# Kernel optimization log

Measured on AMD Instinct MI355X. Metric: run time of the kernel, lower is better.

## Reference

```python
import jax, jax.numpy as jnp
import numpy as np

B, N, K, D = 4096, 64, 48, 64   # batch, n_features, n_bins, d_embedding
F = N * D                        # flattened embedding dim
E, H, O = 8, 1024, 512           # experts, expert hidden, expert out
T, TH = 2, 256                   # tasks, tower hidden


def setup_inputs() -> dict:
    key = jax.random.key(0)
    ks = jax.random.split(key, 10)
    # PLE buffers from uniform bins linspace(0,1,K+1): w = 1/width, b = -edge/width
    edges = jnp.linspace(0.0, 1.0, K + 1)
    width = jnp.diff(edges)
    w = 1.0 / width                      # (K,)
    b = -edges[:-1] / width              # (K,)
    ple_weight = jnp.broadcast_to(w, (N, K)).astype(jnp.float32)
    ple_bias = jnp.broadcast_to(b, (N, K)).astype(jnp.float32)
    s = lambda fan_in: fan_in ** -0.5
    return {
        "x": jax.random.uniform(ks[0], (B, N), jnp.float32),
        "ple_weight": ple_weight,
        "ple_bias": ple_bias,
        "emb_W": jax.random.normal(ks[1], (N, K, D), jnp.float32) * s(K),
        "emb_b": jax.random.normal(ks[2], (N, D), jnp.float32) * s(K),
        "gate_W": jax.random.normal(ks[3], (F, E), jnp.float32) * s(F),
        "gate_b": jnp.zeros((E,), jnp.float32),
        "e_W1": jax.random.normal(ks[4], (E, F, H), jnp.float32) * s(F),
        "e_b1": jnp.zeros((E, H), jnp.float32),
        "e_W2": jax.random.normal(ks[5], (E, H, O), jnp.float32) * s(H),
        "e_b2": jnp.zeros((E, O), jnp.float32),
        "tw1": jax.random.normal(ks[6], (T, O, TH), jnp.float32) * s(O),
        "tb1": jnp.zeros((T, TH), jnp.float32),
        "tw2": jax.random.normal(ks[7], (T, TH, 1), jnp.float32) * s(TH),
        "tb2": jnp.zeros((T, 1), jnp.float32),
        "top_k": 2,
    }


def reference(x, ple_weight, ple_bias, emb_W, emb_b, gate_W, gate_b,
              e_W1, e_b1, e_W2, e_b2, tw1, tb1, tw2, tb2, top_k):
    # --- Piecewise Linear Encoding: (B, N) -> (B, N, K) ---
    enc = ple_bias + ple_weight * x[..., None]
    enc = jnp.concatenate([
        jnp.minimum(enc[..., :1], 1.0),
        jnp.clip(enc[..., 1:-1], 0.0, 1.0),
        jnp.maximum(enc[..., -1:], 0.0),
    ], axis=-1)
    # --- PLE embeddings via NLinear + ReLU: (B, N, K) -> (B, N, D) ---
    emb = jax.nn.relu(jnp.einsum("bnk,nkd->bnd", enc, emb_W) + emb_b)
    flat = emb.reshape(emb.shape[0], -1)                 # (B, F)
    # --- Sparse MoE gating (softmax + top-k renormalized) ---
    probs = jax.nn.softmax(flat @ gate_W + gate_b, axis=-1)   # (B, E)
    topv, topi = jax.lax.top_k(probs, top_k)
    topv = topv / jnp.sum(topv, axis=-1, keepdims=True)
    gates = jnp.zeros_like(probs).at[jnp.arange(probs.shape[0])[:, None], topi].set(topv)
    # --- Experts (computed densely, gated combine) ---
    h = jax.nn.relu(jnp.einsum("bf,efh->beh", flat, e_W1) + e_b1)   # (B, E, H)
    eo = jnp.einsum("beh,eho->beo", h, e_W2) + e_b2                 # (B, E, O)
    moe = jnp.einsum("be,beo->bo", gates, eo)                       # (B, O)
    # --- Task towers: per-task MLP -> scalar ---
    th = jax.nn.relu(jnp.einsum("bo,tos->bts", moe, tw1) + tb1)     # (B, T, TH)
    out = (jnp.einsum("bts,tsu->btu", th, tw2) + tb2)[..., 0]       # (B, T)
    return out
```

## Files before the change

kernel.cpp:

```cpp
#include <hip/hip_runtime.h>
#include <cstdint>

#define B_ 4096
#define N_ 64
#define K_ 48
#define D_ 64
#define F_ 4096
#define E_ 8
#define H_ 1024
#define O_ 512
#define T_ 2
#define TH_ 256
#define NSLOT (B_ * 2)

#define MAXT1 72

typedef float f32x4 __attribute__((ext_vector_type(4)));
typedef __bf16 bf16x8 __attribute__((ext_vector_type(8)));

__device__ __forceinline__ unsigned short f2bf(float f) {
    union { float f; unsigned int u; } v; v.f = f;
    unsigned int u = v.u;
    u += 0x7FFFu + ((u >> 16) & 1u);
    return (unsigned short)(u >> 16);
}

__device__ __forceinline__ void gload_lds16(const void* gptr, void* lptr) {
    auto* g = reinterpret_cast<const __attribute__((address_space(1))) unsigned int*>(
        reinterpret_cast<uintptr_t>(gptr));
    auto* l = reinterpret_cast<__attribute__((address_space(3))) unsigned int*>(
        reinterpret_cast<uintptr_t>(lptr));
    __builtin_amdgcn_global_load_lds(g, l, 16, 0, 0);
}

__global__ __launch_bounds__(64) void prefix_kernel(
    const float* __restrict__ embW, const float* __restrict__ embB,
    float* __restrict__ P)
{
    int n = blockIdx.x;
    int lane = threadIdx.x;
    float acc = embB[n * D_ + lane];
    const float* wsrc = embW + (size_t)n * K_ * D_ + lane;
    float* dst = P + (size_t)n * K_ * D_ + lane;
    #pragma unroll 8
    for (int k = 0; k < K_; ++k) {
        dst[k * D_] = acc;
        acc += wsrc[k * D_];
    }
}

__global__ __launch_bounds__(256) void ple_embed_kernel(
    const float* __restrict__ x, const float* __restrict__ plw,
    const float* __restrict__ plb, const float* __restrict__ embW,
    const float* __restrict__ P, const float* __restrict__ gateW,
    unsigned short* __restrict__ flat_bf, float* __restrict__ logits)
{
    __shared__ float gpart[4][E_];
    int b = blockIdx.x;
    int tid = threadIdx.x, lane = tid & 63, w = tid >> 6;

    float xl = x[b * N_ + lane];
    float gp[E_];
    #pragma unroll
    for (int e = 0; e < E_; ++e) gp[e] = 0.0f;

    #pragma unroll 4
    for (int i = 0; i < 16; ++i) {
        int n = w * 16 + i;
        float xn = __shfl(xl, n);
        const float* pw = plw + n * K_;
        const float* pb = plb + n * K_;
        float t = fmaf(pw[0], xn, pb[0]);
        int j = (int)t;
        j = max(0, min(K_ - 1, j));
        float f = fminf(fmaxf(fmaf(pw[j], xn, pb[j]), 0.0f), 1.0f);
        size_t base = ((size_t)n * K_ + j) * D_ + lane;
        float emb = fmaxf(fmaf(f, embW[base], P[base]), 0.0f);
        flat_bf[(size_t)b * F_ + n * D_ + lane] = f2bf(emb);

        const float4* gw4 = (const float4*)(gateW + (size_t)(n * D_ + lane) * E_);
        float4 g0 = gw4[0], g1 = gw4[1];
        gp[0] = fmaf(emb, g0.x, gp[0]);
        gp[1] = fmaf(emb, g0.y, gp[1]);
        gp[2] = fmaf(emb, g0.z, gp[2]);
        gp[3] = fmaf(emb, g0.w, gp[3]);
        gp[4] = fmaf(emb, g1.x, gp[4]);
        gp[5] = fmaf(emb, g1.y, gp[5]);
        gp[6] = fmaf(emb, g1.z, gp[6]);
        gp[7] = fmaf(emb, g1.w, gp[7]);
    }

    #pragma unroll
    for (int off = 32; off > 0; off >>= 1) {
        #pragma unroll
        for (int e = 0; e < E_; ++e) gp[e] += __shfl_down(gp[e], off);
    }
    if (lane == 0) {
        #pragma unroll
        for (int e = 0; e < E_; ++e) gpart[w][e] = gp[e];
    }
    __syncthreads();
    if (tid < E_)
        logits[b * E_ + tid] =
            gpart[0][tid] + gpart[1][tid] + gpart[2][tid] + gpart[3][tid];
}

__global__ __launch_bounds__(256) void gate_top2_kernel(
    const float* __restrict__ logits, const float* __restrict__ gate_b,
    int* __restrict__ topi, float* __restrict__ topg, int* __restrict__ counts)
{
    int b = blockIdx.x * 256 + threadIdx.x;
    int lane = threadIdx.x & 63;
    float l[E_];
    #pragma unroll
    for (int e = 0; e < E_; ++e) l[e] = logits[b * E_ + e] + gate_b[e];
    int e1 = 0; float v1 = l[0];
    #pragma unroll
    for (int e = 1; e < E_; ++e) if (l[e] > v1) { v1 = l[e]; e1 = e; }
    int e2 = -1; float v2 = -1e30f;
    #pragma unroll
    for (int e = 0; e < E_; ++e) if (e != e1 && l[e] > v2) { v2 = l[e]; e2 = e; }
    float ex = expf(v2 - v1);
    float g1 = 1.0f / (1.0f + ex);
    float g2 = ex / (1.0f + ex);
    topi[b * 2] = e1; topi[b * 2 + 1] = e2;
    topg[b * 2] = g1; topg[b * 2 + 1] = g2;
    #pragma unroll
    for (int e = 0; e < E_; ++e) {
        unsigned long long m1 = __ballot(e1 == e);
        unsigned long long m2 = __ballot(e2 == e);
        if (lane == 0) {
            int c = __popcll(m1) + __popcll(m2);
            if (c) atomicAdd(&counts[e], c);
        }
    }
}

__global__ void scan_kernel(const int* __restrict__ counts, int* __restrict__ offsets,
                            int* __restrict__ tiles1, int* __restrict__ ntiles) {
    int e = threadIdx.x;
    if (e >= E_) return;
    int c[E_];
    #pragma unroll
    for (int i = 0; i < E_; ++i) c[i] = counts[i];
    int off = 0, tb = 0, tot = 0, ttot = 0;
    #pragma unroll
    for (int i = 0; i < E_; ++i) {
        int t = (c[i] + 127) >> 7;
        if (i < e) { off += c[i]; tb += t; }
        tot += c[i]; ttot += t;
    }
    offsets[e] = off;
    if (e == 0) { offsets[E_] = tot; ntiles[0] = ttot; }
    int nt = (c[e] + 127) >> 7;
    for (int tr = 0; tr < nt; ++tr) tiles1[tb + tr] = (e << 16) | tr;
}

__global__ __launch_bounds__(256) void scatter_kernel(
    const int* __restrict__ topi, const float* __restrict__ topg,
    const int* __restrict__ offsets, int* __restrict__ cursors,
    int* __restrict__ rows, float* __restrict__ gatev)
{
    int b = blockIdx.x * 256 + threadIdx.x;
    int lane = threadIdx.x & 63;
    #pragma unroll
    for (int j = 0; j < 2; ++j) {
        int e = topi[b * 2 + j];
        float g = topg[b * 2 + j];
        #pragma unroll
        for (int ex = 0; ex < E_; ++ex) {
            unsigned long long m = __ballot(e == ex);
            if (e == ex) {
                int leader = __builtin_ctzll(m);
                int base = 0;
                if (lane == leader) base = atomicAdd(&cursors[ex], __popcll(m));
                base = __shfl(base, leader);
                int pos = base + __popcll(m & ((1ull << lane) - 1ull));
                int slot = offsets[ex] + pos;
                rows[slot] = b;
                gatev[slot] = g;
            }
        }
    }
}

__global__ __launch_bounds__(256) void wfrag_kernel(
    const float* __restrict__ in, unsigned short* __restrict__ out, int R, int C)
{
    __shared__ float tile[64][65];
    int e = blockIdx.z;
    int rb = blockIdx.x, cb = blockIdx.y;
    const float* src = in + (size_t)e * R * C + (size_t)(rb * 64) * C + cb * 64;
    int lane = threadIdx.x & 63, w = threadIdx.x >> 6;
    #pragma unroll
    for (int i = 0; i < 16; ++i) {
        int r = w * 16 + i;
        tile[r][lane] = src[(size_t)r * C + lane];
    }
    __syncthreads();
    int NB = C >> 4, KB = R >> 5;
    #pragma unroll
    for (int it = 0; it < 2; ++it) {
        int t = threadIdx.x + it * 256;
        int n0r = t >> 7, k0r = (t >> 6) & 1, ln = t & 63;
        int q = ln >> 4, nl = ln & 15;
        unsigned short v[8];
        #pragma unroll
        for (int j = 0; j < 8; ++j)
            v[j] = f2bf(tile[k0r * 32 + q * 8 + j][n0r * 16 + nl]);
        size_t didx = (((size_t)e * NB + cb * 4 + n0r) * KB + rb * 2 + k0r) * 512
                      + (size_t)ln * 8;
        uint4 pk;
        pk.x = v[0] | ((unsigned)v[1] << 16);
        pk.y = v[2] | ((unsigned)v[3] << 16);
        pk.z = v[4] | ((unsigned)v[5] << 16);
        pk.w = v[6] | ((unsigned)v[7] << 16);
        *(uint4*)&out[didx] = pk;
    }
}

__global__ __launch_bounds__(256) void fc1_kernel(
    const unsigned short* __restrict__ Abf,
    const unsigned short* __restrict__ Wf,
    const float* __restrict__ bias,
    const int* __restrict__ rows, const int* __restrict__ offsets,
    const int* __restrict__ tiles1, const int* __restrict__ ntiles,
    unsigned short* __restrict__ Hbf)
{
    int bid = blockIdx.x;
    int tile = bid >> 3, cn = bid & 7;
    if (tile >= ntiles[0]) return;
    int te = tiles1[tile];
    int e = te >> 16, tr = te & 0xffff;
    int m0 = offsets[e], mEnd = offsets[e + 1];
    int Me = mEnd - m0;

    __shared__ alignas(16) unsigned short As[128 * 64];

    int tid = threadIdx.x, lane = tid & 63, wv = tid >> 6;
    int lr = lane >> 3;
    int cg = (lane & 7) ^ lr;

    const unsigned short* aptr[4];
    #pragma unroll
    for (int i = 0; i < 4; ++i) {
        int rowA = (wv * 4 + i) * 8 + lr;
        int slot = min(m0 + tr * 128 + rowA, mEnd - 1);
        aptr[i] = Abf + (size_t)rows[slot] * F_ + cg * 8;
    }

    int wvM = wv >> 1, wvN = wv & 1;
    int m16 = lane & 15, q = lane >> 4;

    const unsigned short* bbase[4];
    #pragma unroll
    for (int nt = 0; nt < 4; ++nt) {
        int n0 = cn * 8 + wvN * 4 + nt;
        bbase[nt] = Wf + (((size_t)e * (H_ / 16) + n0) * (F_ / 32)) * 512
                    + (size_t)lane * 8;
    }

    f32x4 zero = {0.f, 0.f, 0.f, 0.f};
    f32x4 acc[4][4];
    #pragma unroll
    for (int i = 0; i < 4; ++i)
        #pragma unroll
        for (int j = 0; j < 4; ++j) acc[i][j] = zero;

    for (int k0 = 0; k0 < F_; k0 += 64) {
        __syncthreads();
        #pragma unroll
        for (int i = 0; i < 4; ++i)
            gload_lds16(aptr[i] + k0, &As[(wv * 4 + i) * 512]);
        bf16x8 bfr[4][2];
        #pragma unroll
        for (int nt = 0; nt < 4; ++nt)
            #pragma unroll
            for (int ks = 0; ks < 2; ++ks)
                bfr[nt][ks] = *(const bf16x8*)(bbase[nt] + (size_t)k0 * 16 + ks * 512);
        __syncthreads();
        #pragma unroll
        for (int ks = 0; ks < 2; ++ks) {
            bf16x8 af[4];
            #pragma unroll
            for (int mt = 0; mt < 4; ++mt) {
                int m = wvM * 64 + mt * 16 + m16;
                int pos = (ks * 4 + q) ^ (m & 7);
                af[mt] = *(const bf16x8*)&As[m * 64 + pos * 8];
            }
            #pragma unroll
            for (int mt = 0; mt < 4; ++mt)
                #pragma unroll
                for (int nt = 0; nt < 4; ++nt)
                    acc[mt][nt] = __builtin_amdgcn_mfma_f32_16x16x32_bf16(
                        af[mt], bfr[nt][ks], acc[mt][nt], 0, 0, 0);
        }
    }

    #pragma unroll
    for (int nt = 0; nt < 4; ++nt) {
        int col = cn * 128 + wvN * 64 + nt * 16 + m16;
        float bv = bias[e * H_ + col];
        #pragma unroll
        for (int mt = 0; mt < 4; ++mt) {
            int rbase = tr * 128 + wvM * 64 + mt * 16 + q * 4;
            #pragma unroll
            for (int r = 0; r < 4; ++r) {
                int rr = rbase + r;
                if (rr < Me) {
                    float v = fmaxf(acc[mt][nt][r] + bv, 0.0f);
                    Hbf[(size_t)(m0 + rr) * H_ + col] = f2bf(v);
                }
            }
        }
    }
}

__global__ __launch_bounds__(256) void fc2_kernel(
    const unsigned short* __restrict__ Hbf,
    const unsigned short* __restrict__ Wf,
    const float* __restrict__ bias,
    const int* __restrict__ rows, const float* __restrict__ gatev,
    const int* __restrict__ offsets, const int* __restrict__ tiles1,
    const int* __restrict__ ntiles, float* __restrict__ moe)
{
    int bid = blockIdx.x;
    int tile = bid >> 2, cn = bid & 3;
    if (tile >= ntiles[0]) return;
    int te = tiles1[tile];
    int e = te >> 16, tr = te & 0xffff;
    int m0 = offsets[e], mEnd = offsets[e + 1];
    int Me = mEnd - m0;

    __shared__ alignas(16) unsigned short As[128 * 64];

    int tid = threadIdx.x, lane = tid & 63, wv = tid >> 6;
    int lr = lane >> 3;
    int cg = (lane & 7) ^ lr;

    const unsigned short* aptr[4];
    #pragma unroll
    for (int i = 0; i < 4; ++i) {
        int rowA = (wv * 4 + i) * 8 + lr;
        int slot = min(m0 + tr * 128 + rowA, mEnd - 1);
        aptr[i] = Hbf + (size_t)slot * H_ + cg * 8;
    }

    int wvM = wv >> 1, wvN = wv & 1;
    int m16 = lane & 15, q = lane >> 4;

    const unsigned short* bbase[4];
    #pragma unroll
    for (int nt = 0; nt < 4; ++nt) {
        int n0 = cn * 8 + wvN * 4 + nt;
        bbase[nt] = Wf + (((size_t)e * (O_ / 16) + n0) * (H_ / 32)) * 512
                    + (size_t)lane * 8;
    }

    f32x4 zero = {0.f, 0.f, 0.f, 0.f};
    f32x4 acc[4][4];
    #pragma unroll
    for (int i = 0; i < 4; ++i)
        #pragma unroll
        for (int j = 0; j < 4; ++j) acc[i][j] = zero;

    for (int k0 = 0; k0 < H_; k0 += 64) {
        __syncthreads();
        #pragma unroll
        for (int i = 0; i < 4; ++i)
            gload_lds16(aptr[i] + k0, &As[(wv * 4 + i) * 512]);
        bf16x8 bfr[4][2];
        #pragma unroll
        for (int nt = 0; nt < 4; ++nt)
            #pragma unroll
            for (int ks = 0; ks < 2; ++ks)
                bfr[nt][ks] = *(const bf16x8*)(bbase[nt] + (size_t)k0 * 16 + ks * 512);
        __syncthreads();
        #pragma unroll
        for (int ks = 0; ks < 2; ++ks) {
            bf16x8 af[4];
            #pragma unroll
            for (int mt = 0; mt < 4; ++mt) {
                int m = wvM * 64 + mt * 16 + m16;
                int pos = (ks * 4 + q) ^ (m & 7);
                af[mt] = *(const bf16x8*)&As[m * 64 + pos * 8];
            }
            #pragma unroll
            for (int mt = 0; mt < 4; ++mt)
                #pragma unroll
                for (int nt = 0; nt < 4; ++nt)
                    acc[mt][nt] = __builtin_amdgcn_mfma_f32_16x16x32_bf16(
                        af[mt], bfr[nt][ks], acc[mt][nt], 0, 0, 0);
        }
    }

    #pragma unroll
    for (int nt = 0; nt < 4; ++nt) {
        int col = cn * 128 + wvN * 64 + nt * 16 + m16;
        float bv = bias[e * O_ + col];
        #pragma unroll
        for (int mt = 0; mt < 4; ++mt) {
            int rbase = tr * 128 + wvM * 64 + mt * 16 + q * 4;
            #pragma unroll
            for (int r = 0; r < 4; ++r) {
                int rr = rbase + r;
                if (rr < Me) {
                    int slot = m0 + rr;
                    float g = gatev[slot];
                    int b = rows[slot];
                    atomicAdd(&moe[(size_t)b * O_ + col], g * (acc[mt][nt][r] + bv));
                }
            }
        }
    }
}

__global__ __launch_bounds__(256) void tower_kernel(
    const float* __restrict__ moe, const float* __restrict__ tw1,
    const float* __restrict__ tb1, const float* __restrict__ tw2,
    const float* __restrict__ tb2, float* __restrict__ out)
{
    __shared__ float ms[8 * O_];
    __shared__ float red[16][4];
    int b0 = blockIdx.x * 8;
    int tid = threadIdx.x, lane = tid & 63, wv = tid >> 6;
    for (int idx = tid; idx < 8 * O_; idx += 256)
        ms[idx] = moe[(size_t)b0 * O_ + idx];
    __syncthreads();

    int s = tid;
    float a0[8], a1[8];
    float bv0 = tb1[s], bv1 = tb1[TH_ + s];
    #pragma unroll
    for (int i = 0; i < 8; ++i) { a0[i] = bv0; a1[i] = bv1; }

    for (int o = 0; o < O_; o += 4) {
        float w0[4], w1[4];
        #pragma unroll
        for (int u = 0; u < 4; ++u) {
            w0[u] = tw1[(size_t)(o + u) * TH_ + s];
            w1[u] = tw1[(size_t)(O_ + o + u) * TH_ + s];
        }
        #pragma unroll
        for (int i = 0; i < 8; ++i) {
            float4 mv = *(const float4*)&ms[i * O_ + o];
            a0[i] = fmaf(mv.x, w0[0], a0[i]);
            a0[i] = fmaf(mv.y, w0[1], a0[i]);
            a0[i] = fmaf(mv.z, w0[2], a0[i]);
            a0[i] = fmaf(mv.w, w0[3], a0[i]);
            a1[i] = fmaf(mv.x, w1[0], a1[i]);
            a1[i] = fmaf(mv.y, w1[1], a1[i]);
            a1[i] = fmaf(mv.z, w1[2], a1[i]);
            a1[i] = fmaf(mv.w, w1[3], a1[i]);
        }
    }

    float w2a = tw2[s], w2b = tw2[TH_ + s];
    #pragma unroll
    for (int i = 0; i < 8; ++i) {
        float p0 = fmaxf(a0[i], 0.0f) * w2a;
        float p1 = fmaxf(a1[i], 0.0f) * w2b;
        #pragma unroll
        for (int off = 32; off > 0; off >>= 1) {
            p0 += __shfl_down(p0, off);
            p1 += __shfl_down(p1, off);
        }
        if (lane == 0) { red[i * 2 + 0][wv] = p0; red[i * 2 + 1][wv] = p1; }
    }
    __syncthreads();
    if (tid < 16) {
        int i = tid >> 1, t = tid & 1;
        float v = red[tid][0] + red[tid][1] + red[tid][2] + red[tid][3] + tb2[t];
        out[(size_t)(b0 + i) * T_ + t] = v;
    }
}

extern "C" void kernel_launch(void* const* d_in, const int* in_sizes, int n_in,
                              void* d_out, int out_size, void* d_ws, size_t ws_size,
                              hipStream_t stream)
{
    const float* x     = (const float*)d_in[0];
    const float* plw   = (const float*)d_in[1];
    const float* plb   = (const float*)d_in[2];
    const float* embW  = (const float*)d_in[3];
    const float* embB  = (const float*)d_in[4];
    const float* gateW = (const float*)d_in[5];
    const float* gateB = (const float*)d_in[6];
    const float* eW1   = (const float*)d_in[7];
    const float* eB1   = (const float*)d_in[8];
    const float* eW2   = (const float*)d_in[9];
    const float* eB2   = (const float*)d_in[10];
    const float* tw1   = (const float*)d_in[11];
    const float* tb1   = (const float*)d_in[12];
    const float* tw2   = (const float*)d_in[13];
    const float* tb2   = (const float*)d_in[14];
    float* out = (float*)d_out;

    char* w = (char*)d_ws;
    auto alloc = [&](size_t bytes) {
        char* p = w; w += (bytes + 255) & ~(size_t)255; return p;
    };
    unsigned short* flat_bf = (unsigned short*)alloc((size_t)B_ * F_ * 2);
    unsigned short* W1f     = (unsigned short*)alloc((size_t)E_ * H_ * F_ * 2);
    unsigned short* W2f     = (unsigned short*)alloc((size_t)E_ * O_ * H_ * 2);
    unsigned short* Hbf     = (unsigned short*)alloc((size_t)NSLOT * H_ * 2);
    float* Ppre    = (float*)alloc((size_t)N_ * K_ * D_ * 4);
    float* logits  = (float*)alloc((size_t)B_ * E_ * 4);
    float* moe     = (float*)alloc((size_t)B_ * O_ * 4);
    int*   topi    = (int*)alloc((size_t)B_ * 2 * 4);
    float* topg    = (float*)alloc((size_t)B_ * 2 * 4);
    int*   rows    = (int*)alloc((size_t)NSLOT * 4);
    float* gatev   = (float*)alloc((size_t)NSLOT * 4);
    int*   counts  = (int*)alloc(E_ * 4);
    int*   offsets = (int*)alloc((E_ + 1) * 4);
    int*   cursors = (int*)alloc(E_ * 4);
    int*   tiles1  = (int*)alloc(MAXT1 * 4);
    int*   ntiles  = (int*)alloc(2 * 4);

    hipMemsetAsync(moe, 0, (size_t)B_ * O_ * 4, stream);
    hipMemsetAsync(counts, 0, E_ * 4, stream);
    hipMemsetAsync(cursors, 0, E_ * 4, stream);

    prefix_kernel<<<N_, 64, 0, stream>>>(embW, embB, Ppre);
    ple_embed_kernel<<<B_, 256, 0, stream>>>(x, plw, plb, embW, Ppre, gateW,
                                             flat_bf, logits);
    wfrag_kernel<<<dim3(F_ / 64, H_ / 64, E_), 256, 0, stream>>>(eW1, W1f, F_, H_);
    wfrag_kernel<<<dim3(H_ / 64, O_ / 64, E_), 256, 0, stream>>>(eW2, W2f, H_, O_);
    gate_top2_kernel<<<B_ / 256, 256, 0, stream>>>(logits, gateB, topi, topg, counts);
    scan_kernel<<<1, 64, 0, stream>>>(counts, offsets, tiles1, ntiles);
    scatter_kernel<<<B_ / 256, 256, 0, stream>>>(topi, topg, offsets, cursors, rows, gatev);
    fc1_kernel<<<MAXT1 * 8, 256, 0, stream>>>(flat_bf, W1f, eB1, rows, offsets,
                                              tiles1, ntiles, Hbf);
    fc2_kernel<<<MAXT1 * 4, 256, 0, stream>>>(Hbf, W2f, eB2, rows, gatev, offsets,
                                              tiles1, ntiles, moe);
    tower_kernel<<<B_ / 8, 256, 0, stream>>>(moe, tw1, tb1, tw2, tb2, out);
}
```

Baseline: 594.6 us.

## Double-buffer LDS and B-fragment loads in expert FC1/FC2 GEMM kernels

Both expert GEMM kernels now use two LDS buffers for the A tile and two register sets for the B fragments. The next k-slice's global-to-LDS copy and its weight loads are issued before the MFMAs on the current slice, with one barrier per slice instead of two. The aim is to hide global memory latency behind matrix compute. The cost is twice the LDS and more live vector registers, which could lower occupancy.

```diff
diff --git a/kernel.cpp b/kernel.cpp
--- a/kernel.cpp
+++ b/kernel.cpp
@@ -235,7 +235,7 @@
     int m0 = offsets[e], mEnd = offsets[e + 1];
     int Me = mEnd - m0;
 
-    __shared__ alignas(16) unsigned short As[128 * 64];
+    __shared__ alignas(16) unsigned short As[2][128 * 64];
 
     int tid = threadIdx.x, lane = tid & 63, wv = tid >> 6;
     int lr = lane >> 3;
@@ -267,34 +267,56 @@
         #pragma unroll
         for (int j = 0; j < 4; ++j) acc[i][j] = zero;
 
-    for (int k0 = 0; k0 < F_; k0 += 64) {
+#define FC_STAGE(BUF, KK) do {                                              \
+    _Pragma("unroll")                                                       \
+    for (int i_ = 0; i_ < 4; ++i_)                                          \
+        gload_lds16(aptr[i_] + (KK), &As[BUF][(wv * 4 + i_) * 512]);        \
+} while (0)
+
+#define FC_LOADB(DST, KK) do {                                              \
+    _Pragma("unroll")                                                       \
+    for (int nt_ = 0; nt_ < 4; ++nt_)                                       \
+        _Pragma("unroll")                                                   \
+        for (int ks_ = 0; ks_ < 2; ++ks_)                                   \
+            DST[nt_][ks_] = *(const bf16x8*)(bbase[nt_]                     \
+                + (size_t)(KK) * 16 + ks_ * 512);                           \
+} while (0)
+
+#define FC_COMPUTE(BUF, BF) do {                                            \
+    _Pragma("unroll")                                                       \
+    for (int ks_ = 0; ks_ < 2; ++ks_) {                                     \
+        bf16x8 af_[4];                                                      \
+        _Pragma("unroll")                                                   \
+        for (int mt_ = 0; mt_ < 4; ++mt_) {                                 \
+            int m_ = wvM * 64 + mt_ * 16 + m16;                             \
+            int pos_ = (ks_ * 4 + q) ^ (m_ & 7);                            \
+            af_[mt_] = *(const bf16x8*)&As[BUF][m_ * 64 + pos_ * 8];        \
+        }                                                                   \
+        _Pragma("unroll")                                                   \
+        for (int mt_ = 0; mt_ < 4; ++mt_)                                   \
+            _Pragma("unroll")                                               \
+            for (int nt_ = 0; nt_ < 4; ++nt_)                               \
+                acc[mt_][nt_] = __builtin_amdgcn_mfma_f32_16x16x32_bf16(    \
+                    af_[mt_], BF[nt_][ks_], acc[mt_][nt_], 0, 0, 0);        \
+    }                                                                       \
+} while (0)
+
+    bf16x8 bA[4][2], bB[4][2];
+    FC_STAGE(0, 0);
+    FC_LOADB(bA, 0);
+    __syncthreads();
+
+    for (int k0 = 0; k0 < F_; k0 += 128) {
+        FC_STAGE(1, k0 + 64);
+        FC_LOADB(bB, k0 + 64);
+        FC_COMPUTE(0, bA);
         __syncthreads();
-        #pragma unroll
-        for (int i = 0; i < 4; ++i)
-            gload_lds16(aptr[i] + k0, &As[(wv * 4 + i) * 512]);
-        bf16x8 bfr[4][2];
-        #pragma unroll
-        for (int nt = 0; nt < 4; ++nt)
-            #pragma unroll
-            for (int ks = 0; ks < 2; ++ks)
-                bfr[nt][ks] = *(const bf16x8*)(bbase[nt] + (size_t)k0 * 16 + ks * 512);
+        if (k0 + 128 < F_) {
+            FC_STAGE(0, k0 + 128);
+            FC_LOADB(bA, k0 + 128);
+        }
+        FC_COMPUTE(1, bB);
         __syncthreads();
-        #pragma unroll
-        for (int ks = 0; ks < 2; ++ks) {
-            bf16x8 af[4];
-            #pragma unroll
-            for (int mt = 0; mt < 4; ++mt) {
-                int m = wvM * 64 + mt * 16 + m16;
-                int pos = (ks * 4 + q) ^ (m & 7);
-                af[mt] = *(const bf16x8*)&As[m * 64 + pos * 8];
-            }
-            #pragma unroll
-            for (int mt = 0; mt < 4; ++mt)
-                #pragma unroll
-                for (int nt = 0; nt < 4; ++nt)
-                    acc[mt][nt] = __builtin_amdgcn_mfma_f32_16x16x32_bf16(
-                        af[mt], bfr[nt][ks], acc[mt][nt], 0, 0, 0);
-        }
     }
 
     #pragma unroll
@@ -332,7 +354,7 @@
     int m0 = offsets[e], mEnd = offsets[e + 1];
     int Me = mEnd - m0;
 
-    __shared__ alignas(16) unsigned short As[128 * 64];
+    __shared__ alignas(16) unsigned short As[2][128 * 64];
 
     int tid = threadIdx.x, lane = tid & 63, wv = tid >> 6;
     int lr = lane >> 3;
@@ -364,34 +386,22 @@
         #pragma unroll
         for (int j = 0; j < 4; ++j) acc[i][j] = zero;
 
-    for (int k0 = 0; k0 < H_; k0 += 64) {
+    bf16x8 bA[4][2], bB[4][2];
+    FC_STAGE(0, 0);
+    FC_LOADB(bA, 0);
+    __syncthreads();
+
+    for (int k0 = 0; k0 < H_; k0 += 128) {
+        FC_STAGE(1, k0 + 64);
+        FC_LOADB(bB, k0 + 64);
+        FC_COMPUTE(0, bA);
         __syncthreads();
-        #pragma unroll
-        for (int i = 0; i < 4; ++i)
-            gload_lds16(aptr[i] + k0, &As[(wv * 4 + i) * 512]);
-        bf16x8 bfr[4][2];
-        #pragma unroll
-        for (int nt = 0; nt < 4; ++nt)
-            #pragma unroll
-            for (int ks = 0; ks < 2; ++ks)
-                bfr[nt][ks] = *(const bf16x8*)(bbase[nt] + (size_t)k0 * 16 + ks * 512);
+        if (k0 + 128 < H_) {
+            FC_STAGE(0, k0 + 128);
+            FC_LOADB(bA, k0 + 128);
+        }
+        FC_COMPUTE(1, bB);
         __syncthreads();
-        #pragma unroll
-        for (int ks = 0; ks < 2; ++ks) {
-            bf16x8 af[4];
-            #pragma unroll
-            for (int mt = 0; mt < 4; ++mt) {
-                int m = wvM * 64 + mt * 16 + m16;
-                int pos = (ks * 4 + q) ^ (m & 7);
-                af[mt] = *(const bf16x8*)&As[m * 64 + pos * 8];
-            }
-            #pragma unroll
-            for (int mt = 0; mt < 4; ++mt)
-                #pragma unroll
-                for (int nt = 0; nt < 4; ++nt)
-                    acc[mt][nt] = __builtin_amdgcn_mfma_f32_16x16x32_bf16(
-                        af[mt], bfr[nt][ks], acc[mt][nt], 0, 0, 0);
-        }
     }
 
     #pragma unroll
@@ -414,6 +424,10 @@
         }
     }
 }
+
+#undef FC_STAGE
+#undef FC_LOADB
+#undef FC_COMPUTE
 
 __global__ __launch_bounds__(256) void tower_kernel(
     const float* __restrict__ moe, const float* __restrict__ tw1,
```

Result: no change. 584.0 us (-1.8%).
